# Kernel tuning notes

Hardware: AMD Instinct MI355X
Metric: run time of the kernel (lower is better)

The kernel has to match this reference:

```python
import jax, jax.numpy as jnp
import numpy as np

EPS = 1e-8  # cosine-similarity epsilon (torch default)


def setup_inputs() -> dict:
    key = jax.random.key(0)
    k1, k2, k3 = jax.random.split(key, 3)
    B, T, D = 256, 512, 512
    video_embedding = jax.random.normal(k1, (B, T, D), dtype=jnp.float32)
    sentence_embedding = jax.random.normal(k2, (B, D), dtype=jnp.float32)
    # valid lengths in [16, T] so no row is fully masked (softmax stays finite)
    video_lengths = jax.random.randint(k3, (B,), 16, T + 1, dtype=jnp.int32)
    return {
        "video_embedding": video_embedding,
        "sentence_embedding": sentence_embedding,
        "video_lengths": video_lengths,
    }


def reference(video_embedding, sentence_embedding, video_lengths):
    B, T, D = video_embedding.shape
    # cosine similarity between every video frame and every sentence -> [B, B, T]
    vn = video_embedding / jnp.maximum(
        jnp.linalg.norm(video_embedding, axis=-1, keepdims=True), EPS)
    sn = sentence_embedding / jnp.maximum(
        jnp.linalg.norm(sentence_embedding, axis=-1, keepdims=True), EPS)
    sim = jnp.einsum("btd,jd->bjt", vn, sn)  # [B_video, B_sent, T]
    # length mask: frames t >= video_lengths[i] get -inf (vectorized version of
    # the original nested python loop)
    valid = jnp.arange(T)[None, None, :] < video_lengths[:, None, None]  # [B,1,T]
    masked = jnp.where(valid, sim, -jnp.inf)
    similarity = jax.nn.softmax(masked, axis=2)  # [B, B, T]
    # argmax over frames, take the diagonal (matched video/sentence pair)
    max_arg = jnp.argmax(similarity, axis=2)       # [B, B]
    diag = jnp.diagonal(max_arg)                   # [B]
    video_max = jnp.take_along_axis(
        video_embedding, diag[:, None, None], axis=1)[:, 0, :]  # [B, D]
    return similarity, video_max
```

## Files before the change

### kernel.cpp

```cpp
#include <hip/hip_runtime.h>
#include <hip/hip_bf16.h>
#include <cstdint>

constexpr int NB = 256;
constexpr int NT = 512;
constexpr int ND = 512;

typedef __attribute__((ext_vector_type(8))) short bf16x8;
typedef __attribute__((ext_vector_type(4))) float f32x4;
typedef __attribute__((ext_vector_type(4))) unsigned int u32x4;
typedef __attribute__((ext_vector_type(2))) unsigned int u32x2;

__device__ __forceinline__ float wred_sum(float v){
#pragma unroll
  for (int m = 32; m > 0; m >>= 1) v += __shfl_xor(v, m, 64);
  return v;
}
__device__ __forceinline__ unsigned int f2bf(float f){
  unsigned int u = __builtin_bit_cast(unsigned int, f);
  u = u + 0x7fffu + ((u >> 16) & 1u);
  return (u >> 16);
}

__global__ __launch_bounds__(256) void k_sent(const float* __restrict__ s,
                                              unsigned short* __restrict__ sb,
                                              float* __restrict__ sinv){
  int row  = blockIdx.x * 4 + (threadIdx.x >> 6);
  int lane = threadIdx.x & 63;
  const float* sr = s + (size_t)row * ND;
  float x[8]; float ss = 0.f;
#pragma unroll
  for (int e = 0; e < 8; e++){ x[e] = sr[lane + e*64]; ss += x[e]*x[e]; }
  ss = wred_sum(ss);
  float inv = 1.0f / fmaxf(sqrtf(ss), 1e-8f);
#pragma unroll
  for (int e = 0; e < 8; e++)
    sb[(size_t)row*ND + lane + e*64] = (unsigned short)f2bf(x[e]*inv);
  if (lane == 0) sinv[row] = inv;
}

__global__ __launch_bounds__(512, 4) void k_gemm_sm(
    const unsigned short* __restrict__ sb,
    const float* __restrict__ sent,
    const float* __restrict__ sinv,
    const float* __restrict__ video,
    const int* __restrict__ lens,
    float* __restrict__ out0,
    float* __restrict__ diag){
  const int tid  = threadIdx.x;
  const int lane = tid & 63;
  const int w    = tid >> 6;
  const int wj   = w >> 2;
  const int wt   = w & 3;

  const int D  = blockIdx.x;
  const int x8 = D & 7;
  const int r0 = D >> 3;
  const int s  = r0 & 3;
  const int b  = (r0 >> 2) * 8 + x8;
  const int jt = s * 64;

  __shared__ __align__(16) char As[64 * 80];
  __shared__ __align__(16) char Bs[NT * 80];
  __shared__ float sRow[ND];
  __shared__ float vinvS[NT];
  __shared__ float redM[64*4];
  __shared__ float redS[64*4];

  sRow[tid] = sent[(size_t)b*ND + tid];

  const size_t vbase = (size_t)b * NT * ND;
  const float* vsrc  = video + vbase + (size_t)tid * ND;
  const unsigned short* asrc = sb + (size_t)(jt + (tid>>3)) * ND + (tid&7)*4;

  float ssq = 0.f, dtt = 0.f;
  f32x4 acc[2][8] = {};
  f32x4 rb[8];
  u32x2 ra;

#pragma unroll
  for (int i = 0; i < 8; i++) rb[i] = *reinterpret_cast<const f32x4*>(vsrc + i*4);
  ra = *reinterpret_cast<const u32x2*>(asrc);

  char* browp = Bs + tid*80;
  char* arowp = As + (tid>>3)*80 + (tid&7)*8;

  for (int step = 0; step < 16; ++step){
    const int k0 = step * 32;
    __syncthreads();

    {
      float sq = 0.f, dp = 0.f;
#pragma unroll
      for (int i = 0; i < 8; i++){
        f32x4 s4 = *reinterpret_cast<const f32x4*>(&sRow[k0 + i*4]);
#pragma unroll
        for (int j = 0; j < 4; j++){
          float x = rb[i][j];
          sq += x*x; dp += x*s4[j];
        }
      }
      ssq += sq; dtt += dp;
#pragma unroll
      for (int gi = 0; gi < 4; gi++){
        u32x4 d;
        d[0] = f2bf(rb[2*gi  ][0]) | (f2bf(rb[2*gi  ][1]) << 16);
        d[1] = f2bf(rb[2*gi  ][2]) | (f2bf(rb[2*gi  ][3]) << 16);
        d[2] = f2bf(rb[2*gi+1][0]) | (f2bf(rb[2*gi+1][1]) << 16);
        d[3] = f2bf(rb[2*gi+1][2]) | (f2bf(rb[2*gi+1][3]) << 16);
        *reinterpret_cast<u32x4*>(browp + gi*16) = d;
      }
      *reinterpret_cast<u32x2*>(arowp) = ra;
    }

    if (step < 15){
      const int kn = k0 + 32;
#pragma unroll
      for (int i = 0; i < 8; i++) rb[i] = *reinterpret_cast<const f32x4*>(vsrc + kn + i*4);
      ra = *reinterpret_cast<const u32x2*>(asrc + kn);
    }

    __syncthreads();

    {
      const int q  = lane >> 4;
      const int rl = lane & 15;
      bf16x8 af0 = *reinterpret_cast<const bf16x8*>(As + (wj*32 +      rl)*80 + q*16);
      bf16x8 af1 = *reinterpret_cast<const bf16x8*>(As + (wj*32 + 16 + rl)*80 + q*16);
#pragma unroll
      for (int fj = 0; fj < 8; fj++){
        bf16x8 bg = *reinterpret_cast<const bf16x8*>(Bs + (wt*128 + fj*16 + rl)*80 + q*16);
        acc[0][fj] = __builtin_amdgcn_mfma_f32_16x16x32_bf16(af0, bg, acc[0][fj], 0, 0, 0);
        acc[1][fj] = __builtin_amdgcn_mfma_f32_16x16x32_bf16(af1, bg, acc[1][fj], 0, 0, 0);
      }
    }
  }

  {
    float inv = 1.0f / fmaxf(sqrtf(ssq), 1e-8f);
    vinvS[tid] = inv;
    if (jt == 0) diag[(size_t)b*NT + tid] = dtt * inv * sinv[b];
  }
  __syncthreads();

  const int len = lens[b];
  const int q  = lane >> 4;
  const int tl = lane & 15;
  const float NEGINF = -__builtin_inff();

  float mx[2][4];
#pragma unroll
  for (int fi = 0; fi < 2; fi++)
#pragma unroll
    for (int rr = 0; rr < 4; rr++) mx[fi][rr] = NEGINF;

#pragma unroll
  for (int fi = 0; fi < 2; fi++)
#pragma unroll
    for (int fj = 0; fj < 8; fj++){
      int t = wt*128 + fj*16 + tl;
      float vi = vinvS[t];
      bool ok = t < len;
#pragma unroll
      for (int rr = 0; rr < 4; rr++){
        float v = ok ? acc[fi][fj][rr]*vi : NEGINF;
        acc[fi][fj][rr] = v;
        mx[fi][rr] = fmaxf(mx[fi][rr], v);
      }
    }
#pragma unroll
  for (int fi = 0; fi < 2; fi++)
#pragma unroll
    for (int rr = 0; rr < 4; rr++)
#pragma unroll
      for (int msk = 1; msk <= 8; msk <<= 1)
        mx[fi][rr] = fmaxf(mx[fi][rr], __shfl_xor(mx[fi][rr], msk, 64));
  if (tl == 0){
#pragma unroll
    for (int fi = 0; fi < 2; fi++)
#pragma unroll
      for (int rr = 0; rr < 4; rr++)
        redM[(wj*32 + fi*16 + q*4 + rr)*4 + wt] = mx[fi][rr];
  }
  __syncthreads();

  float gmx[2][4], sum[2][4];
#pragma unroll
  for (int fi = 0; fi < 2; fi++)
#pragma unroll
    for (int rr = 0; rr < 4; rr++){
      int jl = wj*32 + fi*16 + q*4 + rr;
      gmx[fi][rr] = fmaxf(fmaxf(redM[jl*4+0], redM[jl*4+1]),
                          fmaxf(redM[jl*4+2], redM[jl*4+3]));
      sum[fi][rr] = 0.f;
    }
#pragma unroll
  for (int fi = 0; fi < 2; fi++)
#pragma unroll
    for (int fj = 0; fj < 8; fj++)
#pragma unroll
      for (int rr = 0; rr < 4; rr++){
        float e = __expf(acc[fi][fj][rr] - gmx[fi][rr]);
        acc[fi][fj][rr] = e;
        sum[fi][rr] += e;
      }
#pragma unroll
  for (int fi = 0; fi < 2; fi++)
#pragma unroll
    for (int rr = 0; rr < 4; rr++)
#pragma unroll
      for (int msk = 1; msk <= 8; msk <<= 1)
        sum[fi][rr] += __shfl_xor(sum[fi][rr], msk, 64);
  if (tl == 0){
#pragma unroll
    for (int fi = 0; fi < 2; fi++)
#pragma unroll
      for (int rr = 0; rr < 4; rr++)
        redS[(wj*32 + fi*16 + q*4 + rr)*4 + wt] = sum[fi][rr];
  }
  __syncthreads();

#pragma unroll
  for (int fi = 0; fi < 2; fi++)
#pragma unroll
    for (int rr = 0; rr < 4; rr++){
      int jl = wj*32 + fi*16 + q*4 + rr;
      float tot = (redS[jl*4+0] + redS[jl*4+1]) + (redS[jl*4+2] + redS[jl*4+3]);
      float iv = 1.0f / tot;
      int j = jt + jl;
      float* orow = out0 + ((size_t)b*NB + j)*NT + wt*128 + tl;
#pragma unroll
      for (int fj = 0; fj < 8; fj++)
        orow[fj*16] = acc[fi][fj][rr]*iv;
    }
}

__global__ __launch_bounds__(256) void k_argmax(const float* __restrict__ video,
                                                const int* __restrict__ lens,
                                                const float* __restrict__ diag,
                                                float* __restrict__ o1){
  int b = blockIdx.x;
  int tid = threadIdx.x;
  int len = lens[b];
  __shared__ float sv[256];
  __shared__ int   si[256];
  const float* dg = diag + (size_t)b * NT;
  float v1 = (tid       < len) ? dg[tid]       : -__builtin_inff();
  float v2 = (tid + 256 < len) ? dg[tid + 256] : -__builtin_inff();
  float bv; int bi;
  if (v2 > v1){ bv = v2; bi = tid + 256; } else { bv = v1; bi = tid; }
  sv[tid] = bv; si[tid] = bi;
  __syncthreads();
  for (int sN = 128; sN > 0; sN >>= 1){
    if (tid < sN){
      float ov = sv[tid+sN]; int oi = si[tid+sN];
      if (ov > sv[tid] || (ov == sv[tid] && oi < si[tid])){ sv[tid] = ov; si[tid] = oi; }
    }
    __syncthreads();
  }
  int best = si[0];
  const float* src = video + ((size_t)b * NT + best) * ND;
  o1[(size_t)b * ND + tid]       = src[tid];
  o1[(size_t)b * ND + tid + 256] = src[tid + 256];
}

extern "C" void kernel_launch(void* const* d_in, const int* in_sizes, int n_in,
                              void* d_out, int out_size, void* d_ws, size_t ws_size,
                              hipStream_t stream){
  const float* video = (const float*)d_in[0];
  const float* sent  = (const float*)d_in[1];
  const int*   lens  = (const int*)d_in[2];
  float* out0 = (float*)d_out;
  float* out1 = out0 + (size_t)NB*NB*NT;

  char* ws = (char*)d_ws;
  unsigned short* sb = (unsigned short*)ws;
  float* sinv  = (float*)(ws + 262144);
  float* diagw = (float*)(ws + 263168);

  k_sent   <<<NB/4, 256, 0, stream>>>(sent, sb, sinv);
  k_gemm_sm<<<NB*4, 512, 0, stream>>>(sb, sent, sinv, video, lens, out0, diagw);
  k_argmax <<<NB,   256, 0, stream>>>(video, lens, diagw, out1);
}
```

Before: 202.8 us.

## Pre-normalize video to bf16 in separate kernel; stage GEMM tiles via direct global-to-LDS loads

Adds a k_vnorm kernel that normalizes each video frame, writes a bf16 copy to workspace and computes the diagonal dot products. The GEMM kernel then loads bf16 tiles straight into double-buffered, XOR-swizzled LDS with global_load_lds, dropping the in-loop fp32→bf16 conversion, the norm accumulation and the per-column scaling. This cuts the GEMM's video reads from fp32 to bf16, since each video tile is re-read by four blocks, and lets loads overlap the MFMAs. The cost is an extra pass that reads the fp32 video once and writes a 128 MB bf16 buffer, plus one more kernel launch.

```diff
diff --git a/kernel.cpp b/kernel.cpp
--- a/kernel.cpp
+++ b/kernel.cpp
@@ -9,7 +9,6 @@
 typedef __attribute__((ext_vector_type(8))) short bf16x8;
 typedef __attribute__((ext_vector_type(4))) float f32x4;
 typedef __attribute__((ext_vector_type(4))) unsigned int u32x4;
-typedef __attribute__((ext_vector_type(2))) unsigned int u32x2;
 
 __device__ __forceinline__ float wred_sum(float v){
 #pragma unroll
@@ -20,6 +19,11 @@
   unsigned int u = __builtin_bit_cast(unsigned int, f);
   u = u + 0x7fffu + ((u >> 16) & 1u);
   return (u >> 16);
+}
+__device__ __forceinline__ void gload_lds16(const void* g, void* l){
+  __builtin_amdgcn_global_load_lds(
+      (const __attribute__((address_space(1))) unsigned int*)g,
+      (__attribute__((address_space(3))) unsigned int*)l, 16, 0, 0);
 }
 
 __global__ __launch_bounds__(256) void k_sent(const float* __restrict__ s,
@@ -39,14 +43,49 @@
   if (lane == 0) sinv[row] = inv;
 }
 
+__global__ __launch_bounds__(256) void k_vnorm(const float* __restrict__ video,
+                                               const float* __restrict__ sent,
+                                               const float* __restrict__ sinv,
+                                               unsigned short* __restrict__ vb16,
+                                               float* __restrict__ diag){
+  const int tid  = threadIdx.x;
+  const int row  = blockIdx.x * 4 + (tid >> 6);
+  const int lane = tid & 63;
+  const int b    = row >> 9;
+  __shared__ float sRowS[ND];
+  sRowS[tid]       = sent[(size_t)b*ND + tid];
+  sRowS[tid + 256] = sent[(size_t)b*ND + 256 + tid];
+  __syncthreads();
+
+  const float* vr = video + (size_t)row * ND;
+  f32x4 x0 = *reinterpret_cast<const f32x4*>(vr + lane*8);
+  f32x4 x1 = *reinterpret_cast<const f32x4*>(vr + lane*8 + 4);
+  float ss = 0.f, dp = 0.f;
+#pragma unroll
+  for (int i = 0; i < 4; i++){
+    ss += x0[i]*x0[i] + x1[i]*x1[i];
+    dp += x0[i]*sRowS[lane*8 + i] + x1[i]*sRowS[lane*8 + 4 + i];
+  }
+#pragma unroll
+  for (int m = 32; m > 0; m >>= 1){
+    ss += __shfl_xor(ss, m, 64);
+    dp += __shfl_xor(dp, m, 64);
+  }
+  float inv = 1.0f / fmaxf(sqrtf(ss), 1e-8f);
+  if (lane == 0) diag[row] = dp * inv * sinv[b];
+  u32x4 d;
+  d[0] = f2bf(x0[0]*inv) | (f2bf(x0[1]*inv) << 16);
+  d[1] = f2bf(x0[2]*inv) | (f2bf(x0[3]*inv) << 16);
+  d[2] = f2bf(x1[0]*inv) | (f2bf(x1[1]*inv) << 16);
+  d[3] = f2bf(x1[2]*inv) | (f2bf(x1[3]*inv) << 16);
+  *reinterpret_cast<u32x4*>(vb16 + (size_t)row*ND + lane*8) = d;
+}
+
 __global__ __launch_bounds__(512, 4) void k_gemm_sm(
     const unsigned short* __restrict__ sb,
-    const float* __restrict__ sent,
-    const float* __restrict__ sinv,
-    const float* __restrict__ video,
+    const unsigned short* __restrict__ vb16,
     const int* __restrict__ lens,
-    float* __restrict__ out0,
-    float* __restrict__ diag){
+    float* __restrict__ out0){
   const int tid  = threadIdx.x;
   const int lane = tid & 63;
   const int w    = tid >> 6;
@@ -60,92 +99,62 @@
   const int b  = (r0 >> 2) * 8 + x8;
   const int jt = s * 64;
 
-  __shared__ __align__(16) char As[64 * 80];
-  __shared__ __align__(16) char Bs[NT * 80];
-  __shared__ float sRow[ND];
-  __shared__ float vinvS[NT];
+  __shared__ __align__(16) unsigned short As[2][64*32];
+  __shared__ __align__(16) unsigned short Bs[2][NT*32];
   __shared__ float redM[64*4];
   __shared__ float redS[64*4];
 
-  sRow[tid] = sent[(size_t)b*ND + tid];
-
-  const size_t vbase = (size_t)b * NT * ND;
-  const float* vsrc  = video + vbase + (size_t)tid * ND;
-  const unsigned short* asrc = sb + (size_t)(jt + (tid>>3)) * ND + (tid&7)*4;
-
-  float ssq = 0.f, dtt = 0.f;
+  const unsigned short* vbase = vb16 + (size_t)b * NT * ND;
+  const int srow = lane >> 2;
+  const int sgr  = ((lane&3) ^ ((lane>>3)&3)) * 8;
+
+  char* AsB = (char*)As;
+  char* BsB = (char*)Bs;
+
+  auto STAGE = [&](int buf, int k0){
+#pragma unroll
+    for (int i = 0; i < 4; i++){
+      int grow = w*64 + i*16 + srow;
+      gload_lds16(vbase + (size_t)grow*ND + k0 + sgr,
+                  BsB + buf*32768 + w*4096 + i*1024 + lane*16);
+    }
+    if (w < 4){
+      int grow = jt + w*16 + srow;
+      gload_lds16(sb + (size_t)grow*ND + k0 + sgr,
+                  AsB + buf*4096 + w*1024 + lane*16);
+    }
+  };
+
   f32x4 acc[2][8] = {};
-  f32x4 rb[8];
-  u32x2 ra;
-
-#pragma unroll
-  for (int i = 0; i < 8; i++) rb[i] = *reinterpret_cast<const f32x4*>(vsrc + i*4);
-  ra = *reinterpret_cast<const u32x2*>(asrc);
-
-  char* browp = Bs + tid*80;
-  char* arowp = As + (tid>>3)*80 + (tid&7)*8;
-
-  for (int step = 0; step < 16; ++step){
-    const int k0 = step * 32;
+
+  STAGE(0, 0);
+  asm volatile("s_waitcnt vmcnt(0)" ::: "memory");
+  __syncthreads();
+
+  const int rl = lane & 15;
+  const int gr = lane >> 4;
+  const int goff = ((gr ^ ((rl>>1)&3)) << 4);
+
+  for (int k = 0; k < 16; ++k){
+    const int cur = k & 1;
+    if (k < 15) STAGE(1-cur, (k+1)*32);
+    __builtin_amdgcn_sched_barrier(0);
+
+    bf16x8 af0 = *reinterpret_cast<const bf16x8*>(AsB + cur*4096 + (wj*32 +      rl)*64 + goff);
+    bf16x8 af1 = *reinterpret_cast<const bf16x8*>(AsB + cur*4096 + (wj*32 + 16 + rl)*64 + goff);
+#pragma unroll
+    for (int fj = 0; fj < 8; fj++){
+      bf16x8 bg = *reinterpret_cast<const bf16x8*>(BsB + cur*32768 + (wt*128 + fj*16 + rl)*64 + goff);
+      acc[0][fj] = __builtin_amdgcn_mfma_f32_16x16x32_bf16(af0, bg, acc[0][fj], 0, 0, 0);
+      acc[1][fj] = __builtin_amdgcn_mfma_f32_16x16x32_bf16(af1, bg, acc[1][fj], 0, 0, 0);
+    }
+    asm volatile("s_waitcnt vmcnt(0)" ::: "memory");
     __syncthreads();
-
-    {
-      float sq = 0.f, dp = 0.f;
-#pragma unroll
-      for (int i = 0; i < 8; i++){
-        f32x4 s4 = *reinterpret_cast<const f32x4*>(&sRow[k0 + i*4]);
-#pragma unroll
-        for (int j = 0; j < 4; j++){
-          float x = rb[i][j];
-          sq += x*x; dp += x*s4[j];
-        }
-      }
-      ssq += sq; dtt += dp;
-#pragma unroll
-      for (int gi = 0; gi < 4; gi++){
-        u32x4 d;
-        d[0] = f2bf(rb[2*gi  ][0]) | (f2bf(rb[2*gi  ][1]) << 16);
-        d[1] = f2bf(rb[2*gi  ][2]) | (f2bf(rb[2*gi  ][3]) << 16);
-        d[2] = f2bf(rb[2*gi+1][0]) | (f2bf(rb[2*gi+1][1]) << 16);
-        d[3] = f2bf(rb[2*gi+1][2]) | (f2bf(rb[2*gi+1][3]) << 16);
-        *reinterpret_cast<u32x4*>(browp + gi*16) = d;
-      }
-      *reinterpret_cast<u32x2*>(arowp) = ra;
-    }
-
-    if (step < 15){
-      const int kn = k0 + 32;
-#pragma unroll
-      for (int i = 0; i < 8; i++) rb[i] = *reinterpret_cast<const f32x4*>(vsrc + kn + i*4);
-      ra = *reinterpret_cast<const u32x2*>(asrc + kn);
-    }
-
-    __syncthreads();
-
-    {
-      const int q  = lane >> 4;
-      const int rl = lane & 15;
-      bf16x8 af0 = *reinterpret_cast<const bf16x8*>(As + (wj*32 +      rl)*80 + q*16);
-      bf16x8 af1 = *reinterpret_cast<const bf16x8*>(As + (wj*32 + 16 + rl)*80 + q*16);
-#pragma unroll
-      for (int fj = 0; fj < 8; fj++){
-        bf16x8 bg = *reinterpret_cast<const bf16x8*>(Bs + (wt*128 + fj*16 + rl)*80 + q*16);
-        acc[0][fj] = __builtin_amdgcn_mfma_f32_16x16x32_bf16(af0, bg, acc[0][fj], 0, 0, 0);
-        acc[1][fj] = __builtin_amdgcn_mfma_f32_16x16x32_bf16(af1, bg, acc[1][fj], 0, 0, 0);
-      }
-    }
-  }
-
-  {
-    float inv = 1.0f / fmaxf(sqrtf(ssq), 1e-8f);
-    vinvS[tid] = inv;
-    if (jt == 0) diag[(size_t)b*NT + tid] = dtt * inv * sinv[b];
-  }
-  __syncthreads();
+  }
 
   const int len = lens[b];
-  const int q  = lane >> 4;
-  const int tl = lane & 15;
+  const int q  = gr;
+  const int tl = rl;
   const float NEGINF = -__builtin_inff();
 
   float mx[2][4];
@@ -159,11 +168,10 @@
 #pragma unroll
     for (int fj = 0; fj < 8; fj++){
       int t = wt*128 + fj*16 + tl;
-      float vi = vinvS[t];
       bool ok = t < len;
 #pragma unroll
       for (int rr = 0; rr < 4; rr++){
-        float v = ok ? acc[fi][fj][rr]*vi : NEGINF;
+        float v = ok ? acc[fi][fj][rr] : NEGINF;
         acc[fi][fj][rr] = v;
         mx[fi][rr] = fmaxf(mx[fi][rr], v);
       }
@@ -274,11 +282,13 @@
   float* out1 = out0 + (size_t)NB*NB*NT;
 
   char* ws = (char*)d_ws;
-  unsigned short* sb = (unsigned short*)ws;
+  unsigned short* sb   = (unsigned short*)ws;
   float* sinv  = (float*)(ws + 262144);
   float* diagw = (float*)(ws + 263168);
-
-  k_sent   <<<NB/4, 256, 0, stream>>>(sent, sb, sinv);
-  k_gemm_sm<<<NB*4, 512, 0, stream>>>(sb, sent, sinv, video, lens, out0, diagw);
-  k_argmax <<<NB,   256, 0, stream>>>(video, lens, diagw, out1);
-}
+  unsigned short* vb16 = (unsigned short*)(ws + 1048576);
+
+  k_sent   <<<NB/4,    256, 0, stream>>>(sent, sb, sinv);
+  k_vnorm  <<<NB*NT/4, 256, 0, stream>>>(video, sent, sinv, vb16, diagw);
+  k_gemm_sm<<<NB*4,    512, 0, stream>>>(sb, vb16, lens, out0);
+  k_argmax <<<NB,      256, 0, stream>>>(video, lens, diagw, out1);
+}
```

Result: faster. 169.0 us (-16.7%).
